# Kernel optimization log

Hardware: AMD Instinct MI355X
Metric: run time of the kernel (lower is better)

The kernel has to match this reference:

```python
import jax, jax.numpy as jnp
import numpy as np

N = 50000
IN_FEAT = 128
HIDDEN = 128
NUM_CLASS = 64
E = 1600000


def setup_inputs() -> dict:
    key = jax.random.key(0)
    ks = jax.random.split(key, 10)
    s = 1.0 / np.sqrt(HIDDEN)
    return {
        "x": jax.random.normal(ks[0], (N, IN_FEAT), dtype=jnp.float32),
        "edge_index": jax.random.randint(ks[1], (2, E), 0, N, dtype=jnp.int64),
        "We": jax.random.uniform(ks[2], (IN_FEAT, HIDDEN), jnp.float32, -s, s),
        "be": jax.random.uniform(ks[3], (HIDDEN,), jnp.float32, -s, s),
        "W1": jax.random.uniform(ks[4], (HIDDEN, HIDDEN), jnp.float32, -s, s),
        "b1": jax.random.uniform(ks[5], (HIDDEN,), jnp.float32, -s, s),
        "W2": jax.random.uniform(ks[6], (HIDDEN, HIDDEN), jnp.float32, -s, s),
        "b2": jax.random.uniform(ks[7], (HIDDEN,), jnp.float32, -s, s),
        "Wo": jax.random.uniform(ks[8], (HIDDEN, NUM_CLASS), jnp.float32, -s, s),
        "bo": jax.random.uniform(ks[9], (NUM_CLASS,), jnp.float32, -s, s),
    }


def _gcn_conv(h, src, dst, norm, W, b, n):
    # h: [N, H]; src/dst/norm: [E+N] (self-loops appended); GCNConv math:
    # out = scatter_add(norm * (h @ W)[src] -> dst) + b
    h = h @ W
    msg = h[src] * norm[:, None]  # gather + scale  [E+N, H]
    out = jax.ops.segment_sum(msg, dst, num_segments=n)
    return out + b


def reference(x, edge_index, We, be, W1, b1, W2, b2, Wo, bo):
    n = x.shape[0]
    loops = jnp.arange(n, dtype=edge_index.dtype)
    src = jnp.concatenate([edge_index[0], loops])
    dst = jnp.concatenate([edge_index[1], loops])
    # symmetric normalization D^{-1/2} (A+I) D^{-1/2}
    deg = jax.ops.segment_sum(jnp.ones_like(dst, dtype=x.dtype), dst, num_segments=n)
    dinv = jnp.where(deg > 0, jax.lax.rsqrt(deg), 0.0)
    norm = dinv[src] * dinv[dst]

    h = x @ We + be                       # encoder
    h = jax.nn.relu(_gcn_conv(h, src, dst, norm, W1, b1, n))
    h = jax.nn.relu(_gcn_conv(h, src, dst, norm, W2, b2, n))
    return h @ Wo + bo                    # decoder
```

## Files before the change

### kernel.cpp

```cpp
#include <hip/hip_runtime.h>
#include <hip/hip_fp16.h>


#define WS_ALIGN(x) (((x) + 255) & ~(size_t)255)
#define RS 100
#define BCHUNK 8192
#define SCHUNKS 8

typedef _Float16 f16x8 __attribute__((ext_vector_type(8)));
typedef float f32x4 __attribute__((ext_vector_type(4)));

__global__ void detect_zero_kernel(const unsigned* __restrict__ p, int* __restrict__ flag,
                                   unsigned* __restrict__ bfil, int nzero) {
    __shared__ int any;
    if (threadIdx.x == 0) any = 0;
    __syncthreads();
    int nz = 0;
    for (int i = threadIdx.x; i < 2048; i += blockDim.x)
        nz |= (p[2 * i + 1] != 0u) ? 1 : 0;
    if (nz) atomicOr(&any, 1);
    for (int i = threadIdx.x; i < nzero; i += blockDim.x) bfil[i] = 0u;
    __syncthreads();
    if (threadIdx.x == 0) *flag = (any == 0) ? 1 : 0;
}

__global__ __launch_bounds__(256) void bucket_kernel(
    const void* __restrict__ ep, const int* __restrict__ flag,
    unsigned* __restrict__ bkt, unsigned* __restrict__ bfill_pad,
    int E, int nbuck, int capB) {
    __shared__ unsigned lcnt[512];
    __shared__ unsigned gcur[512];
    const int tid = threadIdx.x;
    for (int i = tid; i < nbuck; i += 256) lcnt[i] = 0;
    __syncthreads();
    const int base = blockIdx.x * BCHUNK;
    const int end = min(base + BCHUNK, E);
    const int i64 = *flag;
    if (i64) {
        const long long* p = (const long long*)ep;
        for (int i = base + tid; i < end; i += 256) {
            int d = (int)p[(size_t)E + i];
            atomicAdd(&lcnt[d / RS], 1u);
        }
    } else {
        const int* p = (const int*)ep;
        for (int i = base + tid; i < end; i += 256) {
            int d = p[(size_t)E + i];
            atomicAdd(&lcnt[d / RS], 1u);
        }
    }
    __syncthreads();
    for (int i = tid; i < nbuck; i += 256)
        gcur[i] = atomicAdd(&bfill_pad[i << 4], lcnt[i]);
    __syncthreads();
    if (i64) {
        const long long* p = (const long long*)ep;
        for (int i = base + tid; i < end; i += 256) {
            int s = (int)p[i];
            int d = (int)p[(size_t)E + i];
            int part = d / RS;
            int ld = d - part * RS;
            unsigned pos = atomicAdd(&gcur[part], 1u);
            if (pos < (unsigned)capB)
                bkt[(size_t)part * capB + pos] = ((unsigned)ld << 24) | (unsigned)s;
        }
    } else {
        const int* p = (const int*)ep;
        for (int i = base + tid; i < end; i += 256) {
            int s = p[i];
            int d = p[(size_t)E + i];
            int part = d / RS;
            int ld = d - part * RS;
            unsigned pos = atomicAdd(&gcur[part], 1u);
            if (pos < (unsigned)capB)
                bkt[(size_t)part * capB + pos] = ((unsigned)ld << 24) | (unsigned)s;
        }
    }
}

__global__ __launch_bounds__(512) void bucket_scan_kernel(
    const unsigned* __restrict__ bfill_pad, unsigned* __restrict__ ebase,
    int* __restrict__ rowp, int nbuck, int capB, int n) {
    __shared__ unsigned lds[512];
    const int tid = threadIdx.x;
    unsigned v = 0;
    if (tid < nbuck) {
        v = bfill_pad[tid << 4];
        if (v > (unsigned)capB) v = capB;
    }
    lds[tid] = v;
    __syncthreads();
    for (int off = 1; off < 512; off <<= 1) {
        unsigned add = (tid >= off) ? lds[tid - off] : 0;
        __syncthreads();
        lds[tid] += add;
        __syncthreads();
    }
    if (tid < nbuck) ebase[tid] = lds[tid] - v;
    if (tid == 511) rowp[n] = (int)lds[511];
}

__global__ __launch_bounds__(256) void csr_from_bucket_kernel(
    const unsigned* __restrict__ bkt, const unsigned* __restrict__ bfill_pad,
    const unsigned* __restrict__ ebase,
    int* __restrict__ rowp, float* __restrict__ dinv, int* __restrict__ col,
    int capB, int n) {
    __shared__ unsigned hist[RS];
    __shared__ int fillo[RS];
    const int p = blockIdx.x;
    const int tid = threadIdx.x;
    for (int i = tid; i < RS; i += 256) hist[i] = 0;
    __syncthreads();
    unsigned cnt = bfill_pad[p << 4];
    if (cnt > (unsigned)capB) cnt = capB;
    const unsigned* bp = bkt + (size_t)p * capB;
    for (unsigned e = tid; e < cnt; e += 256)
        atomicAdd(&hist[bp[e] >> 24], 1u);
    __syncthreads();
    if (tid == 0) {
        int run = (int)ebase[p];
        for (int i = 0; i < RS; ++i) { fillo[i] = run; run += (int)hist[i]; }
    }
    __syncthreads();
    const int lo = p * RS;
    for (int i = tid; i < RS; i += 256) {
        int node = lo + i;
        if (node < n) {
            rowp[node] = fillo[i];
            dinv[node] = rsqrtf((float)(hist[i] + 1u));
        }
    }
    __syncthreads();
    const int csz = (n + SCHUNKS - 1) / SCHUNKS;
#pragma unroll 1
    for (int q = 0; q < SCHUNKS; ++q) {
        int lo_s = q * csz;
        int hi_s = lo_s + csz;
        for (unsigned e = tid; e < cnt; e += 256) {
            unsigned u = bp[e];
            int s = (int)(u & 0xFFFFFFu);
            if (s >= lo_s && s < hi_s) {
                int ld = (int)(u >> 24);
                int pos = atomicAdd(&fillo[ld], 1);
                col[pos] = s;
            }
        }
        __syncthreads();
    }
}

__global__ __launch_bounds__(256) void wcomb_kernel(
    const float* __restrict__ We, const float* __restrict__ W1,
    const float* __restrict__ be, float* __restrict__ Wcomb,
    float* __restrict__ bcomb) {
    int t = blockIdx.x * 256 + threadIdx.x;
    int r = t >> 7, c = t & 127;
    float s = 0.f;
    for (int k = 0; k < 128; ++k) s = fmaf(We[r * 128 + k], W1[k * 128 + c], s);
    Wcomb[t] = s;
    if (t < 128) {
        float b = 0.f;
        for (int k = 0; k < 128; ++k) b = fmaf(be[k], W1[k * 128 + t], b);
        bcomb[t] = b;
    }
}

__global__ __launch_bounds__(256) void wfrag3_kernel(
    const float* __restrict__ Wa, __half* __restrict__ WaF,
    const float* __restrict__ Wb, __half* __restrict__ WbF,
    const float* __restrict__ Wc, __half* __restrict__ WcF, int nco) {
    const float* W;
    __half* Wf;
    int ncol, t;
    if (blockIdx.x < 8)       { W = Wa; Wf = WaF; ncol = 128; t = blockIdx.x * 256 + threadIdx.x; }
    else if (blockIdx.x < 16) { W = Wb; Wf = WbF; ncol = 128; t = (blockIdx.x - 8) * 256 + threadIdx.x; }
    else                      { W = Wc; Wf = WcF; ncol = nco; t = (blockIdx.x - 16) * 256 + threadIdx.x; }
    int total = (ncol >> 4) * 4 * 64;
    if (t >= total) return;
    int lane = t & 63;
    int ks = (t >> 6) & 3;
    int c0 = t >> 8;
    int colw = c0 * 16 + (lane & 15);
    int k0 = ks * 32 + ((lane >> 4) << 3);
    __half vals[8];
#pragma unroll
    for (int j = 0; j < 8; ++j) vals[j] = __float2half(W[(size_t)(k0 + j) * ncol + colw]);
    *(uint4*)(Wf + (size_t)t * 8) = *(uint4*)vals;
}

__device__ __forceinline__ void h8_acc(uint4 r, float* a) {
    float2 f;
    f = __half22float2(*(const __half2*)&r.x); a[0] += f.x; a[1] += f.y;
    f = __half22float2(*(const __half2*)&r.y); a[2] += f.x; a[3] += f.y;
    f = __half22float2(*(const __half2*)&r.z); a[4] += f.x; a[5] += f.y;
    f = __half22float2(*(const __half2*)&r.w); a[6] += f.x; a[7] += f.y;
}

__global__ __launch_bounds__(256) void agg_pull_kernel(
    const int* __restrict__ rowp, const int* __restrict__ col,
    const float* __restrict__ dinv, const __half* __restrict__ t,
    const float* __restrict__ bias, __half* __restrict__ out, int n) {
    int node = blockIdx.x * 16 + (threadIdx.x >> 4);
    int lane = threadIdx.x & 15;
    if (node >= n) return;
    const uint4* T = (const uint4*)t;
    int j0 = rowp[node], j1 = rowp[node + 1];
    float dn = dinv[node];

    float acc[8] = {0.f, 0.f, 0.f, 0.f, 0.f, 0.f, 0.f, 0.f};
    h8_acc(T[(size_t)node * 16 + lane], acc);

    int j = j0;
    for (; j + 7 < j1; j += 8) {
        int c[8];
        uint4 r[8];
#pragma unroll
        for (int k = 0; k < 8; ++k) c[k] = col[j + k];
#pragma unroll
        for (int k = 0; k < 8; ++k) r[k] = T[(size_t)c[k] * 16 + lane];
#pragma unroll
        for (int k = 0; k < 8; ++k) h8_acc(r[k], acc);
    }
    for (; j + 3 < j1; j += 4) {
        int c[4];
        uint4 r[4];
#pragma unroll
        for (int k = 0; k < 4; ++k) c[k] = col[j + k];
#pragma unroll
        for (int k = 0; k < 4; ++k) r[k] = T[(size_t)c[k] * 16 + lane];
#pragma unroll
        for (int k = 0; k < 4; ++k) h8_acc(r[k], acc);
    }
    for (; j < j1; ++j) h8_acc(T[(size_t)col[j] * 16 + lane], acc);

    const float4* B4 = (const float4*)bias;
    float4 ba = B4[lane * 2 + 0];
    float4 bb = B4[lane * 2 + 1];
    float o0 = fmaxf(fmaf(acc[0], dn, ba.x), 0.f);
    float o1 = fmaxf(fmaf(acc[1], dn, ba.y), 0.f);
    float o2 = fmaxf(fmaf(acc[2], dn, ba.z), 0.f);
    float o3 = fmaxf(fmaf(acc[3], dn, ba.w), 0.f);
    float o4 = fmaxf(fmaf(acc[4], dn, bb.x), 0.f);
    float o5 = fmaxf(fmaf(acc[5], dn, bb.y), 0.f);
    float o6 = fmaxf(fmaf(acc[6], dn, bb.z), 0.f);
    float o7 = fmaxf(fmaf(acc[7], dn, bb.w), 0.f);
    __half2 h0 = __floats2half2_rn(o0, o1);
    __half2 h1 = __floats2half2_rn(o2, o3);
    __half2 h2 = __floats2half2_rn(o4, o5);
    __half2 h3 = __floats2half2_rn(o6, o7);
    uint4 packed;
    packed.x = *(unsigned*)&h0;
    packed.y = *(unsigned*)&h1;
    packed.z = *(unsigned*)&h2;
    packed.w = *(unsigned*)&h3;
    ((uint4*)out)[(size_t)node * 16 + lane] = packed;
}

__device__ __forceinline__ f16x8 frag_from_f32(const float* p) {
    float4 u = *(const float4*)p;
    float4 v = *(const float4*)(p + 4);
    f16x8 r;
    r[0] = (_Float16)u.x; r[1] = (_Float16)u.y; r[2] = (_Float16)u.z; r[3] = (_Float16)u.w;
    r[4] = (_Float16)v.x; r[5] = (_Float16)v.y; r[6] = (_Float16)v.z; r[7] = (_Float16)v.w;
    return r;
}

__global__ __launch_bounds__(256) void gemm_mfma_kernel(
    const void* __restrict__ A, const __half* __restrict__ Wf,
    const float* __restrict__ bias, const float* __restrict__ rowscale,
    void* __restrict__ C, int n, int ncol, int a_fp32, int c_fp32) {
    const int wave = threadIdx.x >> 6;
    const int lane = threadIdx.x & 63;
    const int row0 = blockIdx.x * 64 + wave * 16;
    int ar = row0 + (lane & 15);
    if (ar >= n) ar = n - 1;
    const int koff = (lane >> 4) << 3;
    f16x8 a0, a1, a2, a3;
    if (a_fp32) {
        const float* ab = (const float*)A + (size_t)ar * 128 + koff;
        a0 = frag_from_f32(ab);
        a1 = frag_from_f32(ab + 32);
        a2 = frag_from_f32(ab + 64);
        a3 = frag_from_f32(ab + 96);
    } else {
        const __half* ab = (const __half*)A + (size_t)ar * 128 + koff;
        a0 = *(const f16x8*)(ab);
        a1 = *(const f16x8*)(ab + 32);
        a2 = *(const f16x8*)(ab + 64);
        a3 = *(const f16x8*)(ab + 96);
    }
    const int ncc = ncol >> 4;
    const int cic = lane & 15;
    const int rbase = (lane >> 4) << 2;
    float rs[4];
#pragma unroll
    for (int r = 0; r < 4; ++r) {
        int row = row0 + rbase + r;
        rs[r] = (rowscale && row < n) ? rowscale[row] : 1.f;
    }
    for (int c0 = 0; c0 < ncc; ++c0) {
        const f16x8* wf = (const f16x8*)Wf + (size_t)c0 * 256 + lane;
        f32x4 acc = {0.f, 0.f, 0.f, 0.f};
        acc = __builtin_amdgcn_mfma_f32_16x16x32_f16(a0, wf[0],   acc, 0, 0, 0);
        acc = __builtin_amdgcn_mfma_f32_16x16x32_f16(a1, wf[64],  acc, 0, 0, 0);
        acc = __builtin_amdgcn_mfma_f32_16x16x32_f16(a2, wf[128], acc, 0, 0, 0);
        acc = __builtin_amdgcn_mfma_f32_16x16x32_f16(a3, wf[192], acc, 0, 0, 0);
        int colc = (c0 << 4) + cic;
        float bv = bias ? bias[colc] : 0.f;
#pragma unroll
        for (int r = 0; r < 4; ++r) {
            int row = row0 + rbase + r;
            if (row < n) {
                float v = (acc[r] + bv) * rs[r];
                if (c_fp32) ((float*)C)[(size_t)row * ncol + colc] = v;
                else        ((__half*)C)[(size_t)row * ncol + colc] = __float2half(v);
            }
        }
    }
}

extern "C" void kernel_launch(void* const* d_in, const int* in_sizes, int n_in,
                              void* d_out, int out_size, void* d_ws, size_t ws_size,
                              hipStream_t stream) {
    const float* x  = (const float*)d_in[0];
    const void*  ei = d_in[1];
    const float* We = (const float*)d_in[2];
    const float* be = (const float*)d_in[3];
    const float* W1 = (const float*)d_in[4];
    const float* b1 = (const float*)d_in[5];
    const float* W2 = (const float*)d_in[6];
    const float* b2 = (const float*)d_in[7];
    const float* Wo = (const float*)d_in[8];
    const float* bo = (const float*)d_in[9];
    const int N = in_sizes[0] / 128;
    const int E = in_sizes[1] / 2;
    const int NC = in_sizes[9];
    const int nbuck = (N + RS - 1) / RS;
    const int capB = (E + nbuck - 1) / nbuck + 512;

    char* ws = (char*)d_ws;
    size_t off = 0;
    int*      flag = (int*)(ws + off);      off += 256;
    unsigned* bfil = (unsigned*)(ws + off); off += WS_ALIGN((size_t)nbuck * 64);
    unsigned* ebas = (unsigned*)(ws + off); off += WS_ALIGN((size_t)nbuck * 4);
    unsigned* bkt  = (unsigned*)(ws + off); off += WS_ALIGN((size_t)nbuck * capB * 4);
    float*    dinv = (float*)(ws + off);    off += WS_ALIGN((size_t)N * 4);
    int*      rowp = (int*)(ws + off);      off += WS_ALIGN((size_t)(N + 1) * 4);
    int*      colw = (int*)(ws + off);      off += WS_ALIGN((size_t)E * 4);
    float*    Wcmb = (float*)(ws + off);    off += WS_ALIGN((size_t)128 * 128 * 4);
    float*    bcmb = (float*)(ws + off);    off += WS_ALIGN((size_t)128 * 4);
    __half*   WcF  = (__half*)(ws + off);   off += WS_ALIGN((size_t)128 * 128 * 2);
    __half*   W2F  = (__half*)(ws + off);   off += WS_ALIGN((size_t)128 * 128 * 2);
    __half*   WoF  = (__half*)(ws + off);   off += WS_ALIGN((size_t)128 * 64 * 2);
    __half*   hA   = (__half*)(ws + off);   off += WS_ALIGN((size_t)N * 128 * 2);
    __half*   tH   = (__half*)(ws + off);   off += WS_ALIGN((size_t)N * 128 * 2);

    const int nb_bucket = (E + BCHUNK - 1) / BCHUNK;
    dim3 blk(256);

    detect_zero_kernel<<<1, 256, 0, stream>>>((const unsigned*)ei, flag, bfil, nbuck * 16);
    bucket_kernel<<<nb_bucket, blk, 0, stream>>>(ei, flag, bkt, bfil, E, nbuck, capB);
    bucket_scan_kernel<<<1, 512, 0, stream>>>(bfil, ebas, rowp, nbuck, capB, N);
    csr_from_bucket_kernel<<<nbuck, blk, 0, stream>>>(bkt, bfil, ebas, rowp, dinv, colw, capB, N);

    wcomb_kernel<<<64, blk, 0, stream>>>(We, W1, be, Wcmb, bcmb);
    wfrag3_kernel<<<20, blk, 0, stream>>>(Wcmb, WcF, W2, W2F, Wo, WoF, NC);

    const int gemm_blocks = (N + 63) / 64;
    const int agg_blocks = (N + 15) / 16;

    gemm_mfma_kernel<<<gemm_blocks, blk, 0, stream>>>(x, WcF, bcmb, dinv, tH, N, 128, 1, 0);
    agg_pull_kernel<<<agg_blocks, blk, 0, stream>>>(rowp, colw, dinv, tH, b1, hA, N);
    gemm_mfma_kernel<<<gemm_blocks, blk, 0, stream>>>(hA, W2F, nullptr, dinv, tH, N, 128, 0, 0);
    agg_pull_kernel<<<agg_blocks, blk, 0, stream>>>(rowp, colw, dinv, tH, b2, hA, N);
    gemm_mfma_kernel<<<gemm_blocks, blk, 0, stream>>>(hA, WoF, bo, nullptr, d_out, N, NC, 0, 1);
}
```

Before: 224.5 us.

## Fold bucket scan into CSR build, fuse weight combine with fragment packing

```diff
diff --git a/kernel.cpp b/kernel.cpp
--- a/kernel.cpp
+++ b/kernel.cpp
@@ -5,7 +5,6 @@
 #define WS_ALIGN(x) (((x) + 255) & ~(size_t)255)
 #define RS 100
 #define BCHUNK 8192
-#define SCHUNKS 8
 
 typedef _Float16 f16x8 __attribute__((ext_vector_type(8)));
 typedef float f32x4 __attribute__((ext_vector_type(4)));
@@ -78,39 +77,28 @@
     }
 }
 
-__global__ __launch_bounds__(512) void bucket_scan_kernel(
-    const unsigned* __restrict__ bfill_pad, unsigned* __restrict__ ebase,
-    int* __restrict__ rowp, int nbuck, int capB, int n) {
-    __shared__ unsigned lds[512];
-    const int tid = threadIdx.x;
-    unsigned v = 0;
-    if (tid < nbuck) {
-        v = bfill_pad[tid << 4];
-        if (v > (unsigned)capB) v = capB;
-    }
-    lds[tid] = v;
-    __syncthreads();
-    for (int off = 1; off < 512; off <<= 1) {
-        unsigned add = (tid >= off) ? lds[tid - off] : 0;
-        __syncthreads();
-        lds[tid] += add;
-        __syncthreads();
-    }
-    if (tid < nbuck) ebase[tid] = lds[tid] - v;
-    if (tid == 511) rowp[n] = (int)lds[511];
-}
-
 __global__ __launch_bounds__(256) void csr_from_bucket_kernel(
     const unsigned* __restrict__ bkt, const unsigned* __restrict__ bfill_pad,
-    const unsigned* __restrict__ ebase,
     int* __restrict__ rowp, float* __restrict__ dinv, int* __restrict__ col,
-    int capB, int n) {
+    int capB, int n, int nbuck) {
     __shared__ unsigned hist[RS];
     __shared__ int fillo[RS];
+    __shared__ unsigned wsum[4];
+    __shared__ unsigned ebase_sh;
     const int p = blockIdx.x;
     const int tid = threadIdx.x;
+
+    unsigned s = 0;
+    for (int q = tid; q < p; q += 256) {
+        unsigned c = bfill_pad[q << 4];
+        s += (c > (unsigned)capB) ? (unsigned)capB : c;
+    }
+    for (int o = 32; o; o >>= 1) s += __shfl_down(s, o, 64);
+    if ((tid & 63) == 0) wsum[tid >> 6] = s;
     for (int i = tid; i < RS; i += 256) hist[i] = 0;
     __syncthreads();
+    if (tid == 0) ebase_sh = wsum[0] + wsum[1] + wsum[2] + wsum[3];
+
     unsigned cnt = bfill_pad[p << 4];
     if (cnt > (unsigned)capB) cnt = capB;
     const unsigned* bp = bkt + (size_t)p * capB;
@@ -118,8 +106,9 @@
         atomicAdd(&hist[bp[e] >> 24], 1u);
     __syncthreads();
     if (tid == 0) {
-        int run = (int)ebase[p];
+        int run = (int)ebase_sh;
         for (int i = 0; i < RS; ++i) { fillo[i] = run; run += (int)hist[i]; }
+        if (p == nbuck - 1) rowp[n] = run;
     }
     __syncthreads();
     const int lo = p * RS;
@@ -131,50 +120,55 @@
         }
     }
     __syncthreads();
-    const int csz = (n + SCHUNKS - 1) / SCHUNKS;
-#pragma unroll 1
-    for (int q = 0; q < SCHUNKS; ++q) {
-        int lo_s = q * csz;
-        int hi_s = lo_s + csz;
-        for (unsigned e = tid; e < cnt; e += 256) {
-            unsigned u = bp[e];
-            int s = (int)(u & 0xFFFFFFu);
-            if (s >= lo_s && s < hi_s) {
-                int ld = (int)(u >> 24);
-                int pos = atomicAdd(&fillo[ld], 1);
-                col[pos] = s;
-            }
+    for (unsigned e = tid; e < cnt; e += 256) {
+        unsigned u = bp[e];
+        int ld = (int)(u >> 24);
+        int pos = atomicAdd(&fillo[ld], 1);
+        col[pos] = (int)(u & 0xFFFFFFu);
+    }
+}
+
+__global__ __launch_bounds__(256) void wfrag3_kernel(
+    const float* __restrict__ We, const float* __restrict__ W1,
+    const float* __restrict__ be, float* __restrict__ bcomb,
+    __half* __restrict__ WcF,
+    const float* __restrict__ W2, __half* __restrict__ W2F,
+    const float* __restrict__ Wo, __half* __restrict__ WoF, int nco) {
+    const int tid = threadIdx.x;
+    if (blockIdx.x < 8) {
+        __shared__ float tile[128 * 16];
+        const int c0 = blockIdx.x;
+        for (int i = tid; i < 128 * 16; i += 256) {
+            int k = i >> 4, cc = i & 15;
+            int colw = c0 * 16 + cc;
+            float acc = 0.f;
+            for (int m = 0; m < 128; ++m)
+                acc = fmaf(We[k * 128 + m], W1[m * 128 + colw], acc);
+            tile[i] = acc;
         }
         __syncthreads();
-    }
-}
-
-__global__ __launch_bounds__(256) void wcomb_kernel(
-    const float* __restrict__ We, const float* __restrict__ W1,
-    const float* __restrict__ be, float* __restrict__ Wcomb,
-    float* __restrict__ bcomb) {
-    int t = blockIdx.x * 256 + threadIdx.x;
-    int r = t >> 7, c = t & 127;
-    float s = 0.f;
-    for (int k = 0; k < 128; ++k) s = fmaf(We[r * 128 + k], W1[k * 128 + c], s);
-    Wcomb[t] = s;
-    if (t < 128) {
-        float b = 0.f;
-        for (int k = 0; k < 128; ++k) b = fmaf(be[k], W1[k * 128 + t], b);
-        bcomb[t] = b;
-    }
-}
-
-__global__ __launch_bounds__(256) void wfrag3_kernel(
-    const float* __restrict__ Wa, __half* __restrict__ WaF,
-    const float* __restrict__ Wb, __half* __restrict__ WbF,
-    const float* __restrict__ Wc, __half* __restrict__ WcF, int nco) {
+        if (tid < 16) {
+            int colw = c0 * 16 + tid;
+            float b = 0.f;
+            for (int m = 0; m < 128; ++m) b = fmaf(be[m], W1[m * 128 + colw], b);
+            bcomb[colw] = b;
+        }
+        int t = c0 * 256 + tid;
+        int lane = t & 63;
+        int ks = (t >> 6) & 3;
+        __half vals[8];
+        int cc = lane & 15;
+        int k0 = ks * 32 + ((lane >> 4) << 3);
+#pragma unroll
+        for (int j = 0; j < 8; ++j) vals[j] = __float2half(tile[(k0 + j) * 16 + cc]);
+        *(uint4*)(WcF + (size_t)t * 8) = *(uint4*)vals;
+        return;
+    }
     const float* W;
     __half* Wf;
     int ncol, t;
-    if (blockIdx.x < 8)       { W = Wa; Wf = WaF; ncol = 128; t = blockIdx.x * 256 + threadIdx.x; }
-    else if (blockIdx.x < 16) { W = Wb; Wf = WbF; ncol = 128; t = (blockIdx.x - 8) * 256 + threadIdx.x; }
-    else                      { W = Wc; Wf = WcF; ncol = nco; t = (blockIdx.x - 16) * 256 + threadIdx.x; }
+    if (blockIdx.x < 16) { W = W2; Wf = W2F; ncol = 128; t = (blockIdx.x - 8) * 256 + tid; }
+    else                 { W = Wo; Wf = WoF; ncol = nco; t = (blockIdx.x - 16) * 256 + tid; }
     int total = (ncol >> 4) * 4 * 64;
     if (t >= total) return;
     int lane = t & 63;
@@ -342,12 +336,10 @@
     size_t off = 0;
     int*      flag = (int*)(ws + off);      off += 256;
     unsigned* bfil = (unsigned*)(ws + off); off += WS_ALIGN((size_t)nbuck * 64);
-    unsigned* ebas = (unsigned*)(ws + off); off += WS_ALIGN((size_t)nbuck * 4);
     unsigned* bkt  = (unsigned*)(ws + off); off += WS_ALIGN((size_t)nbuck * capB * 4);
     float*    dinv = (float*)(ws + off);    off += WS_ALIGN((size_t)N * 4);
     int*      rowp = (int*)(ws + off);      off += WS_ALIGN((size_t)(N + 1) * 4);
     int*      colw = (int*)(ws + off);      off += WS_ALIGN((size_t)E * 4);
-    float*    Wcmb = (float*)(ws + off);    off += WS_ALIGN((size_t)128 * 128 * 4);
     float*    bcmb = (float*)(ws + off);    off += WS_ALIGN((size_t)128 * 4);
     __half*   WcF  = (__half*)(ws + off);   off += WS_ALIGN((size_t)128 * 128 * 2);
     __half*   W2F  = (__half*)(ws + off);   off += WS_ALIGN((size_t)128 * 128 * 2);
@@ -360,11 +352,9 @@
 
     detect_zero_kernel<<<1, 256, 0, stream>>>((const unsigned*)ei, flag, bfil, nbuck * 16);
     bucket_kernel<<<nb_bucket, blk, 0, stream>>>(ei, flag, bkt, bfil, E, nbuck, capB);
-    bucket_scan_kernel<<<1, 512, 0, stream>>>(bfil, ebas, rowp, nbuck, capB, N);
-    csr_from_bucket_kernel<<<nbuck, blk, 0, stream>>>(bkt, bfil, ebas, rowp, dinv, colw, capB, N);
-
-    wcomb_kernel<<<64, blk, 0, stream>>>(We, W1, be, Wcmb, bcmb);
-    wfrag3_kernel<<<20, blk, 0, stream>>>(Wcmb, WcF, W2, W2F, Wo, WoF, NC);
+    csr_from_bucket_kernel<<<nbuck, blk, 0, stream>>>(bkt, bfil, rowp, dinv, colw, capB, N, nbuck);
+
+    wfrag3_kernel<<<20, blk, 0, stream>>>(We, W1, be, bcmb, WcF, W2, W2F, Wo, WoF, NC);
 
     const int gemm_blocks = (N + 63) / 64;
     const int agg_blocks = (N + 15) / 16;
```

Result: slower. 235.4 us (+4.9%).
